# Optimization experiments

Hardware: AMD Instinct MI355X
Metric: run time of the kernel (lower is better)

The kernel has to match this reference:

```python
import jax, jax.numpy as jnp
import numpy as np


def setup_inputs() -> dict:
    key = jax.random.key(0)
    ks = jax.random.split(key, 16)
    B, S, H = 512, 128, 256
    f32 = jnp.float32
    inputs = jax.random.normal(ks[0], (B, S, 2), f32)
    # xavier-normal-ish init (gain/sqrt(fan_in+fan_out) approximated by small scale)
    def xn(k, shape):
        fan = shape[0] + shape[1]
        return jax.random.normal(k, shape, f32) * np.sqrt(2.0 / fan)
    return {
        "inputs": inputs,
        "W0": xn(ks[1], (H, 2)),   "b0": jnp.zeros((H,), f32),
        "W1": xn(ks[2], (H, H)),   "b1": jnp.zeros((H,), f32),
        "W2": xn(ks[3], (H, H)),   "b2": jnp.zeros((H,), f32),
        "W3": xn(ks[4], (H, H)),   "b3": jnp.zeros((H,), f32),
        "W4": xn(ks[5], (1, H)),   "b4": jnp.zeros((1,), f32),
        "log_growth_rate": jax.random.normal(ks[6], (), f32),
        "log_carrying_capacity": jax.random.normal(ks[7], (), f32),
        "log_initial_loss": jax.random.normal(ks[8], (), f32),
        "in_mean": jnp.array([0.5, 50.0], f32),
        "in_std": jnp.array([0.2, 30.0], f32),
        "tgt_mean": jnp.array([0.8], f32),
        "tgt_std": jnp.array([0.1], f32),
    }


def reference(inputs, W0, b0, W1, b1, W2, b2, W3, b3, W4, b4,
              log_growth_rate, log_carrying_capacity, log_initial_loss,
              in_mean, in_std, tgt_mean, tgt_std):
    B, S = inputs.shape[0], inputs.shape[1]
    # PDE parameters (Verhulst logistic growth)
    r = jnp.exp(-log_growth_rate)
    K = 0.2 + (1.0 - 0.2) * jax.nn.sigmoid(log_carrying_capacity)  # carrying capacity in [0.2, 1]
    C = 0.0 + (0.1 - 0.0) * jax.nn.sigmoid(log_initial_loss)       # initial loss in [0, 0.1]

    # split state feature s and time t, standardize per-column
    s = inputs[..., 0:1].reshape(-1, 1)  # [N,1]
    t = inputs[..., 1:2].reshape(-1, 1)  # [N,1]
    s_norm = (s - in_mean[0:1]) / (in_std[0:1] + 1e-8)
    t_norm = (t - in_mean[1:2]) / (in_std[1:2] + 1e-8)

    Ws = (W0, W1, W2, W3, W4)
    bs = (b0, b1, b2, b3, b4)

    def mlp(x):  # [N,2] -> [N,1], tanh MLP
        h = x
        for W, b in zip(Ws[:-1], bs[:-1]):
            h = jnp.tanh(h @ W.T + b)
        return h @ Ws[-1].T + bs[-1]

    def u_of(tn):  # U(s_norm, tn), inverse-standardized targets
        return mlp(jnp.concatenate([s_norm, tn], axis=-1)) * tgt_std + tgt_mean

    ones = jnp.ones_like(t_norm)

    def uf_of(tn):
        # U and U_t = dU/dt_norm (forward-mode; each point depends on its own scalar t)
        U, U_dot = jax.jvp(u_of, (tn,), (ones,))
        U_t = U_dot.sum(-1, keepdims=True)
        G = r * (U - C) * (1.0 - (U - C) / (K - C))  # Verhulst
        return U, U_t - G  # (U, F)

    # second derivative w.r.t. t_norm: F_t = U_tt - G_t
    (U, F), (_, F_t) = jax.jvp(uf_of, (t_norm,), (ones,))

    shp = (B, S, 1)
    return U.reshape(shp), F.reshape(shp), F_t.reshape(shp)
```

## Files before the change

### kernel.cpp

```cpp
#include <hip/hip_runtime.h>
#include <hip/hip_bf16.h>
#include <math.h>

typedef short s8v __attribute__((ext_vector_type(8)));
typedef float f4v __attribute__((ext_vector_type(4)));

#define HH 256
#define TP 64
#define NTHREADS 256
#define NGRP 4
#define KSTR 520
#define TSTR 4160
#define NTILES 12
#define PLANE (NTILES * TSTR)

__device__ __forceinline__ unsigned short bf_rne(float x){
    union{float f;unsigned u;}v; v.f=x;
    unsigned r = v.u + 0x7FFFu + ((v.u >> 16) & 1u);
    return (unsigned short)(r >> 16);
}
__device__ __forceinline__ unsigned pack_rne2(float a, float b){
    union { __hip_bfloat162 h; unsigned u; } v;
    v.h = __float22bfloat162_rn(float2{a, b});
    return v.u;
}

__global__ __launch_bounds__(256)
void prep_weights(const float* __restrict__ W1, const float* __restrict__ W2,
                  const float* __restrict__ W3, const float* __restrict__ W0,
                  const float* __restrict__ b0, const float* __restrict__ W4,
                  unsigned short* __restrict__ wsB, float* __restrict__ wsF)
{
    int t = blockIdx.x * 256 + threadIdx.x;
    if (t < 24576) {
        int layer = t >> 13;
        int rem = t & 8191;
        int l  = rem & 63;
        int ks = (rem >> 6) & 7;
        int nt = rem >> 9;
        const float* W = (layer == 0) ? W1 : (layer == 1) ? W2 : W3;
        int n_out = nt * 16 + (l & 15);
        int quad  = l >> 4;
        const float* row = W + n_out * HH;
        s8v hi;
        #pragma unroll
        for (int j = 0; j < 8; ++j) {
            int n_in = quad * 64 + (j & 3) * 16 + ((j >> 2) << 3) + ks;
            hi[j] = (short)bf_rne(row[n_in]);
        }
        int dst = ((nt * 8 + ks) * 64 + l) * 8;
        *(s8v*)(wsB + layer * 65536 + dst) = hi;
    } else if (t < 24832) {
        int n = t - 24576;
        int pos = ((n & 7) * 4 + (n >> 6)) * 8 + ((n >> 4) & 3) + 4 * ((n >> 3) & 1);
        wsF[pos]       = W0[2 * n];
        wsF[256 + pos] = W0[2 * n + 1];
        wsF[512 + pos] = b0[n];
        wsF[768 + pos] = W4[n];
    }
}

template<int H>
__device__ __forceinline__ void mfma_group(
    f4v (&acc)[3][4], const s8v (&Bv)[4][8],
    const unsigned short* Ahi, const float* __restrict__ bL,
    int lane, int w, int m16)
{
    #pragma unroll
    for (int i = 0; i < 4; ++i) {
        float bias = bL[w * 64 + i * 16 + m16];
        acc[0][i] = (f4v){bias, bias, bias, bias};
        acc[1][i] = (f4v){0.f, 0.f, 0.f, 0.f};
        acc[2][i] = (f4v){0.f, 0.f, 0.f, 0.f};
    }
    __builtin_amdgcn_s_setprio(1);
    #pragma unroll
    for (int ks = 0; ks < 8; ++ks) {
        const int aoff = ks * KSTR + lane * 8;
        s8v a0 = *(const s8v*)&Ahi[(0 * NGRP + H) * TSTR + aoff];
        s8v a1 = *(const s8v*)&Ahi[(1 * NGRP + H) * TSTR + aoff];
        s8v a2 = *(const s8v*)&Ahi[(2 * NGRP + H) * TSTR + aoff];
        #pragma unroll
        for (int i = 0; i < 4; ++i) {
            acc[0][i] = __builtin_amdgcn_mfma_f32_16x16x32_bf16(a0, Bv[i][ks], acc[0][i], 0, 0, 0);
            acc[1][i] = __builtin_amdgcn_mfma_f32_16x16x32_bf16(a1, Bv[i][ks], acc[1][i], 0, 0, 0);
            acc[2][i] = __builtin_amdgcn_mfma_f32_16x16x32_bf16(a2, Bv[i][ks], acc[2][i], 0, 0, 0);
        }
    }
    __builtin_amdgcn_s_setprio(0);
}

template<int H>
__device__ __forceinline__ void transform_group(
    f4v (&acc)[3][4], unsigned short* Ahi, int w, int m16, int q)
{
    const int ksw  = m16 & 7;
    const int hsel = m16 >> 3;
    const int wbase = ksw * KSTR + (16 * w + q * 4) * 8 + 4 * hsel;
    #pragma unroll
    for (int r = 0; r < 4; ++r) {
        float Av[3][4];
        #pragma unroll
        for (int i = 0; i < 4; ++i) {
            float z  = acc[0][i][r];
            float z1 = acc[1][i][r];
            float z2 = acc[2][i][r];
            float e = __expf(2.f * z);
            float a = 1.f - 2.f * __builtin_amdgcn_rcpf(e + 1.f);
            float g = 1.f - a * a;
            float d1 = g * z1;
            float d2 = fmaf(g, z2, -2.f * a * d1 * z1);
            Av[0][i] = a; Av[1][i] = d1; Av[2][i] = d2;
        }
        #pragma unroll
        for (int s = 0; s < 3; ++s) {
            int2 hi2;
            hi2.x = (int)pack_rne2(Av[s][0], Av[s][1]);
            hi2.y = (int)pack_rne2(Av[s][2], Av[s][3]);
            *(int2*)&Ahi[(s * NGRP + H) * TSTR + wbase + r * 8] = hi2;
        }
    }
}

template<int H>
__device__ __forceinline__ void head_group(
    f4v (&acc)[3][4], const float (&w4v)[4], float* head_part,
    int w, int m16, int q)
{
    float hp[3][4];
    #pragma unroll
    for (int s = 0; s < 3; ++s)
        #pragma unroll
        for (int r = 0; r < 4; ++r) hp[s][r] = 0.f;
    #pragma unroll
    for (int r = 0; r < 4; ++r) {
        #pragma unroll
        for (int i = 0; i < 4; ++i) {
            float z  = acc[0][i][r];
            float z1 = acc[1][i][r];
            float z2 = acc[2][i][r];
            float e = __expf(2.f * z);
            float a = 1.f - 2.f * __builtin_amdgcn_rcpf(e + 1.f);
            float g = 1.f - a * a;
            float d1 = g * z1;
            float d2 = fmaf(g, z2, -2.f * a * d1 * z1);
            hp[0][r] = fmaf(w4v[i], a,  hp[0][r]);
            hp[1][r] = fmaf(w4v[i], d1, hp[1][r]);
            hp[2][r] = fmaf(w4v[i], d2, hp[2][r]);
        }
    }
    #pragma unroll
    for (int m = 1; m < 16; m <<= 1) {
        #pragma unroll
        for (int s = 0; s < 3; ++s)
            #pragma unroll
            for (int r = 0; r < 4; ++r)
                hp[s][r] += __shfl_xor(hp[s][r], m);
    }
    if (m16 == 0) {
        #pragma unroll
        for (int s = 0; s < 3; ++s)
            #pragma unroll
            for (int r = 0; r < 4; ++r)
                head_part[(s * TP + H * 16 + q * 4 + r) * 4 + w] = hp[s][r];
    }
}

#define LOADB(Wlh)                                                          \
    do {                                                                    \
        _Pragma("unroll")                                                   \
        for (int i = 0; i < 4; ++i)                                         \
            _Pragma("unroll")                                               \
            for (int ks = 0; ks < 8; ++ks)                                  \
                Bv[i][ks] = *(const s8v*)((Wlh) +                           \
                    (((w * 4 + i) * 8 + ks) * 64 + lane) * 8);              \
    } while (0)

__global__ __launch_bounds__(NTHREADS, 1)
void capnn_mfma(const float* __restrict__ inp,
                const float* __restrict__ b1, const float* __restrict__ b2,
                const float* __restrict__ b3, const float* __restrict__ b4,
                const float* __restrict__ W4raw,
                const float* __restrict__ lgr, const float* __restrict__ lcc,
                const float* __restrict__ lil,
                const float* __restrict__ imean, const float* __restrict__ istd,
                const float* __restrict__ tmean, const float* __restrict__ tstd,
                const unsigned short* __restrict__ wsW,
                const float* __restrict__ wsF,
                float* __restrict__ out, int N)
{
    __shared__ __align__(16) unsigned short Ahi[PLANE];
    __shared__ float sn_sh[TP], tn_sh[TP];
    __shared__ float head_part[TP * 3 * 4];

    const int tid  = threadIdx.x;
    const int lane = tid & 63;
    const int w    = tid >> 6;
    const int m16  = lane & 15;
    const int q    = lane >> 4;
    const int pbase = blockIdx.x * TP;

    const float* __restrict__ w00p = wsF;
    const float* __restrict__ w01p = wsF + 256;
    const float* __restrict__ b0p  = wsF + 512;

    if (tid < TP) {
        int pg = pbase + tid;
        float s = 0.f, t = 0.f;
        if (pg < N) { s = inp[2 * pg]; t = inp[2 * pg + 1]; }
        sn_sh[tid] = (s - imean[0]) / (istd[0] + 1e-8f);
        tn_sh[tid] = (t - imean[1]) / (istd[1] + 1e-8f);
    }
    __syncthreads();

    {
        const int l  = lane;
        const int p16 = l & 15, quad = l >> 4;
        #pragma unroll
        for (int g2 = 0; g2 < 2; ++g2) {
            const int ks = w + 4 * g2;
            const int pos = (ks * 4 + quad) * 8;
            float4 wA0 = *(const float4*)(w00p + pos);
            float4 wA1 = *(const float4*)(w00p + pos + 4);
            float4 wB0 = *(const float4*)(w01p + pos);
            float4 wB1 = *(const float4*)(w01p + pos + 4);
            float4 bb0 = *(const float4*)(b0p + pos);
            float4 bb1 = *(const float4*)(b0p + pos + 4);
            float w00v[8] = {wA0.x,wA0.y,wA0.z,wA0.w,wA1.x,wA1.y,wA1.z,wA1.w};
            float w01v[8] = {wB0.x,wB0.y,wB0.z,wB0.w,wB1.x,wB1.y,wB1.z,wB1.w};
            float b0v[8]  = {bb0.x,bb0.y,bb0.z,bb0.w,bb1.x,bb1.y,bb1.z,bb1.w};
            const int base = ks * KSTR + l * 8;
            #pragma unroll
            for (int h = 0; h < NGRP; ++h) {
                const float sn = sn_sh[h * 16 + p16], tn = tn_sh[h * 16 + p16];
                float av[8], d1v[8], d2v[8];
                #pragma unroll
                for (int j = 0; j < 8; ++j) {
                    float z = fmaf(w00v[j], sn, fmaf(w01v[j], tn, b0v[j]));
                    float e = __expf(2.f * z);
                    float a = 1.f - 2.f * __builtin_amdgcn_rcpf(e + 1.f);
                    float g = 1.f - a * a;
                    float d1 = g * w01v[j];
                    float d2 = -2.f * a * d1 * w01v[j];
                    av[j] = a; d1v[j] = d1; d2v[j] = d2;
                }
                #pragma unroll
                for (int s = 0; s < 3; ++s) {
                    const float* V = (s == 0) ? av : (s == 1) ? d1v : d2v;
                    int4 hi4;
                    hi4.x = (int)pack_rne2(V[0], V[1]);
                    hi4.y = (int)pack_rne2(V[2], V[3]);
                    hi4.z = (int)pack_rne2(V[4], V[5]);
                    hi4.w = (int)pack_rne2(V[6], V[7]);
                    *(int4*)&Ahi[(s * NGRP + h) * TSTR + base] = hi4;
                }
            }
        }
    }
    __syncthreads();

    f4v accA[3][4], accB[3][4];
    s8v Bv[4][8];
    const unsigned short* __restrict__ W1h = wsW;
    const unsigned short* __restrict__ W2h = wsW + 65536;
    const unsigned short* __restrict__ W3h = wsW + 131072;

    LOADB(W1h);
    mfma_group<0>(accA, Bv, Ahi, b1, lane, w, m16);
    __syncthreads();
    mfma_group<1>(accB, Bv, Ahi, b1, lane, w, m16);
    transform_group<0>(accA, Ahi, w, m16, q);
    __syncthreads();
    mfma_group<2>(accA, Bv, Ahi, b1, lane, w, m16);
    transform_group<1>(accB, Ahi, w, m16, q);
    __syncthreads();
    mfma_group<3>(accB, Bv, Ahi, b1, lane, w, m16);
    transform_group<2>(accA, Ahi, w, m16, q);
    __syncthreads();
    transform_group<3>(accB, Ahi, w, m16, q);

    LOADB(W2h);
    mfma_group<0>(accA, Bv, Ahi, b2, lane, w, m16);
    __syncthreads();
    mfma_group<1>(accB, Bv, Ahi, b2, lane, w, m16);
    transform_group<0>(accA, Ahi, w, m16, q);
    __syncthreads();
    mfma_group<2>(accA, Bv, Ahi, b2, lane, w, m16);
    transform_group<1>(accB, Ahi, w, m16, q);
    __syncthreads();
    mfma_group<3>(accB, Bv, Ahi, b2, lane, w, m16);
    transform_group<2>(accA, Ahi, w, m16, q);
    __syncthreads();
    transform_group<3>(accB, Ahi, w, m16, q);

    LOADB(W3h);
    float w4v[4];
    #pragma unroll
    for (int i = 0; i < 4; ++i) w4v[i] = W4raw[w * 64 + i * 16 + m16];

    mfma_group<0>(accA, Bv, Ahi, b3, lane, w, m16);
    __syncthreads();
    mfma_group<1>(accB, Bv, Ahi, b3, lane, w, m16);
    head_group<0>(accA, w4v, head_part, w, m16, q);
    __syncthreads();
    mfma_group<2>(accA, Bv, Ahi, b3, lane, w, m16);
    head_group<1>(accB, w4v, head_part, w, m16, q);
    __syncthreads();
    mfma_group<3>(accB, Bv, Ahi, b3, lane, w, m16);
    head_group<2>(accA, w4v, head_part, w, m16, q);
    __syncthreads();
    head_group<3>(accB, w4v, head_part, w, m16, q);
    __syncthreads();

    if (tid < TP) {
        float sv = 0.f, s1v = 0.f, s2v = 0.f;
        #pragma unroll
        for (int ww = 0; ww < 4; ++ww) {
            sv  += head_part[(0 * TP + tid) * 4 + ww];
            s1v += head_part[(1 * TP + tid) * 4 + ww];
            s2v += head_part[(2 * TP + tid) * 4 + ww];
        }
        int pg = pbase + tid;
        if (pg < N) {
            float r_  = expf(-lgr[0]);
            float Kc  = 0.2f + 0.8f / (1.f + expf(-lcc[0]));
            float Cc  = 0.1f / (1.f + expf(-lil[0]));
            float kci = 1.f / (Kc - Cc);
            float ts = tstd[0], tm = tmean[0];
            float U   = (sv + b4[0]) * ts + tm;
            float Ut  = s1v * ts;
            float Utt = s2v * ts;
            float Um  = U - Cc;
            float G   = r_ * Um * (1.f - Um * kci);
            float Gt  = r_ * Ut * (1.f - 2.f * Um * kci);
            out[pg]         = U;
            out[N + pg]     = Ut - G;
            out[2 * N + pg] = Utt - Gt;
        }
    }
}

extern "C" void kernel_launch(void* const* d_in, const int* in_sizes, int n_in,
                              void* d_out, int out_size, void* d_ws, size_t ws_size,
                              hipStream_t stream) {
    const float* inp   = (const float*)d_in[0];
    const float* W0    = (const float*)d_in[1];
    const float* b0    = (const float*)d_in[2];
    const float* W1    = (const float*)d_in[3];
    const float* b1    = (const float*)d_in[4];
    const float* W2    = (const float*)d_in[5];
    const float* b2    = (const float*)d_in[6];
    const float* W3    = (const float*)d_in[7];
    const float* b3    = (const float*)d_in[8];
    const float* W4    = (const float*)d_in[9];
    const float* b4    = (const float*)d_in[10];
    const float* lgr   = (const float*)d_in[11];
    const float* lcc   = (const float*)d_in[12];
    const float* lil   = (const float*)d_in[13];
    const float* imean = (const float*)d_in[14];
    const float* istd  = (const float*)d_in[15];
    const float* tmean = (const float*)d_in[16];
    const float* tstd  = (const float*)d_in[17];

    unsigned short* wsB = (unsigned short*)d_ws;
    float* wsF = (float*)((char*)d_ws + 393216);

    const int N = in_sizes[0] / 2;
    const int gridMain = (N + TP - 1) / TP;

    hipLaunchKernelGGL(prep_weights, dim3(97), dim3(256), 0, stream,
                       W1, W2, W3, W0, b0, W4, wsB, wsF);
    hipLaunchKernelGGL(capnn_mfma, dim3(gridMain), dim3(NTHREADS), 0, stream,
                       inp, b1, b2, b3, b4, W4,
                       lgr, lcc, lil, imean, istd, tmean, tstd,
                       wsB, wsF, (float*)d_out, N);
}
```

Baseline: 196.7 us.

## Halve points per block to fit two blocks per CU and restructure pipeline

```diff
diff --git a/kernel.cpp b/kernel.cpp
--- a/kernel.cpp
+++ b/kernel.cpp
@@ -6,12 +6,11 @@
 typedef float f4v __attribute__((ext_vector_type(4)));
 
 #define HH 256
-#define TP 64
+#define TP 32
 #define NTHREADS 256
-#define NGRP 4
 #define KSTR 520
 #define TSTR 4160
-#define NTILES 12
+#define NTILES 6
 #define PLANE (NTILES * TSTR)
 
 __device__ __forceinline__ unsigned short bf_rne(float x){
@@ -77,9 +76,9 @@
     #pragma unroll
     for (int ks = 0; ks < 8; ++ks) {
         const int aoff = ks * KSTR + lane * 8;
-        s8v a0 = *(const s8v*)&Ahi[(0 * NGRP + H) * TSTR + aoff];
-        s8v a1 = *(const s8v*)&Ahi[(1 * NGRP + H) * TSTR + aoff];
-        s8v a2 = *(const s8v*)&Ahi[(2 * NGRP + H) * TSTR + aoff];
+        s8v a0 = *(const s8v*)&Ahi[(0 + H) * TSTR + aoff];
+        s8v a1 = *(const s8v*)&Ahi[(2 + H) * TSTR + aoff];
+        s8v a2 = *(const s8v*)&Ahi[(4 + H) * TSTR + aoff];
         #pragma unroll
         for (int i = 0; i < 4; ++i) {
             acc[0][i] = __builtin_amdgcn_mfma_f32_16x16x32_bf16(a0, Bv[i][ks], acc[0][i], 0, 0, 0);
@@ -117,7 +116,7 @@
             int2 hi2;
             hi2.x = (int)pack_rne2(Av[s][0], Av[s][1]);
             hi2.y = (int)pack_rne2(Av[s][2], Av[s][3]);
-            *(int2*)&Ahi[(s * NGRP + H) * TSTR + wbase + r * 8] = hi2;
+            *(int2*)&Ahi[(s * 2 + H) * TSTR + wbase + r * 8] = hi2;
         }
     }
 }
@@ -176,7 +175,7 @@
                     (((w * 4 + i) * 8 + ks) * 64 + lane) * 8);              \
     } while (0)
 
-__global__ __launch_bounds__(NTHREADS, 1)
+__global__ __launch_bounds__(NTHREADS, 2)
 void capnn_mfma(const float* __restrict__ inp,
                 const float* __restrict__ b1, const float* __restrict__ b2,
                 const float* __restrict__ b3, const float* __restrict__ b4,
@@ -211,6 +210,13 @@
         sn_sh[tid] = (s - imean[0]) / (istd[0] + 1e-8f);
         tn_sh[tid] = (t - imean[1]) / (istd[1] + 1e-8f);
     }
+
+    s8v Bv[4][8];
+    const unsigned short* __restrict__ W1h = wsW;
+    const unsigned short* __restrict__ W2h = wsW + 65536;
+    const unsigned short* __restrict__ W3h = wsW + 131072;
+    LOADB(W1h);
+
     __syncthreads();
 
     {
@@ -231,7 +237,7 @@
             float b0v[8]  = {bb0.x,bb0.y,bb0.z,bb0.w,bb1.x,bb1.y,bb1.z,bb1.w};
             const int base = ks * KSTR + l * 8;
             #pragma unroll
-            for (int h = 0; h < NGRP; ++h) {
+            for (int h = 0; h < 2; ++h) {
                 const float sn = sn_sh[h * 16 + p16], tn = tn_sh[h * 16 + p16];
                 float av[8], d1v[8], d2v[8];
                 #pragma unroll
@@ -252,7 +258,7 @@
                     hi4.y = (int)pack_rne2(V[2], V[3]);
                     hi4.z = (int)pack_rne2(V[4], V[5]);
                     hi4.w = (int)pack_rne2(V[6], V[7]);
-                    *(int4*)&Ahi[(s * NGRP + h) * TSTR + base] = hi4;
+                    *(int4*)&Ahi[(s * 2 + h) * TSTR + base] = hi4;
                 }
             }
         }
@@ -260,56 +266,33 @@
     __syncthreads();
 
     f4v accA[3][4], accB[3][4];
-    s8v Bv[4][8];
-    const unsigned short* __restrict__ W1h = wsW;
-    const unsigned short* __restrict__ W2h = wsW + 65536;
-    const unsigned short* __restrict__ W3h = wsW + 131072;
-
-    LOADB(W1h);
+
     mfma_group<0>(accA, Bv, Ahi, b1, lane, w, m16);
     __syncthreads();
     mfma_group<1>(accB, Bv, Ahi, b1, lane, w, m16);
     transform_group<0>(accA, Ahi, w, m16, q);
     __syncthreads();
-    mfma_group<2>(accA, Bv, Ahi, b1, lane, w, m16);
+
+    LOADB(W2h);
     transform_group<1>(accB, Ahi, w, m16, q);
-    __syncthreads();
-    mfma_group<3>(accB, Bv, Ahi, b1, lane, w, m16);
-    transform_group<2>(accA, Ahi, w, m16, q);
-    __syncthreads();
-    transform_group<3>(accB, Ahi, w, m16, q);
-
-    LOADB(W2h);
     mfma_group<0>(accA, Bv, Ahi, b2, lane, w, m16);
     __syncthreads();
+
     mfma_group<1>(accB, Bv, Ahi, b2, lane, w, m16);
     transform_group<0>(accA, Ahi, w, m16, q);
     __syncthreads();
-    mfma_group<2>(accA, Bv, Ahi, b2, lane, w, m16);
-    transform_group<1>(accB, Ahi, w, m16, q);
-    __syncthreads();
-    mfma_group<3>(accB, Bv, Ahi, b2, lane, w, m16);
-    transform_group<2>(accA, Ahi, w, m16, q);
-    __syncthreads();
-    transform_group<3>(accB, Ahi, w, m16, q);
 
     LOADB(W3h);
     float w4v[4];
     #pragma unroll
     for (int i = 0; i < 4; ++i) w4v[i] = W4raw[w * 64 + i * 16 + m16];
-
+    transform_group<1>(accB, Ahi, w, m16, q);
     mfma_group<0>(accA, Bv, Ahi, b3, lane, w, m16);
     __syncthreads();
+
     mfma_group<1>(accB, Bv, Ahi, b3, lane, w, m16);
     head_group<0>(accA, w4v, head_part, w, m16, q);
-    __syncthreads();
-    mfma_group<2>(accA, Bv, Ahi, b3, lane, w, m16);
     head_group<1>(accB, w4v, head_part, w, m16, q);
-    __syncthreads();
-    mfma_group<3>(accB, Bv, Ahi, b3, lane, w, m16);
-    head_group<2>(accA, w4v, head_part, w, m16, q);
-    __syncthreads();
-    head_group<3>(accB, w4v, head_part, w, m16, q);
     __syncthreads();
 
     if (tid < TP) {
```

Measured after the change: 215.8 us. +9.7%, slower.
